# Kernel tuning notes

Measured on AMD Instinct MI355X. Metric: run time of the kernel, lower is better.

## Reference

```python
import jax, jax.numpy as jnp
import numpy as np

B, IN, H, OUT, E = 8192, 1024, 4096, 1024, 8
HG = H // 2  # gating hidden

def setup_inputs() -> dict:
    key = jax.random.key(0)
    ks = jax.random.split(key, 9)
    s_in = 1.0 / np.sqrt(IN)
    s_h = 1.0 / np.sqrt(H)
    s_hg = 1.0 / np.sqrt(HG)
    return {
        "x": jax.random.normal(ks[0], (B, IN), jnp.float32),
        # gating MLP: Linear(IN,HG) -> ReLU -> Linear(HG,E) -> softmax
        "gw1": jax.random.uniform(ks[1], (IN, HG), jnp.float32, -s_in, s_in),
        "gb1": jax.random.uniform(ks[2], (HG,), jnp.float32, -s_in, s_in),
        "gw2": jax.random.uniform(ks[3], (HG, E), jnp.float32, -s_hg, s_hg),
        "gb2": jax.random.uniform(ks[4], (E,), jnp.float32, -s_hg, s_hg),
        # experts: E x (Linear(IN,H) -> ReLU -> Linear(H,OUT))
        "ew1": jax.random.uniform(ks[5], (E, IN, H), jnp.float32, -s_in, s_in),
        "eb1": jax.random.uniform(ks[6], (E, H), jnp.float32, -s_in, s_in),
        "ew2": jax.random.uniform(ks[7], (E, H, OUT), jnp.float32, -s_h, s_h),
        "eb2": jax.random.uniform(ks[8], (E, OUT), jnp.float32, -s_h, s_h),
    }

def reference(x, gw1, gb1, gw2, gb2, ew1, eb1, ew2, eb2):
    # Gating network (dropout is a no-op in eval)
    gh = jax.nn.relu(x @ gw1 + gb1)                       # [B, HG]
    gates = jax.nn.softmax(gh @ gw2 + gb2, axis=1)        # [B, E]
    # All experts run on the full batch
    h = jax.nn.relu(jnp.einsum('bi,eih->beh', x, ew1) + eb1[None])  # [B, E, H]
    eo = jnp.einsum('beh,eho->beo', h, ew2) + eb2[None]             # [B, E, OUT]
    # Gate-weighted combine: (stacked * gates[...,None]).sum(dim=1)
    combined = jnp.einsum('beo,be->bo', eo, gates)        # [B, OUT]
    return combined
```

## Files before the change

### kernel.cpp

```cpp
#include <hip/hip_runtime.h>


#define DI __device__ __forceinline__

typedef _Float16 f16;
typedef _Float16 f16x8 __attribute__((ext_vector_type(8)));
typedef float f32x4 __attribute__((ext_vector_type(4)));

constexpr int BSZ  = 8192;
constexpr int IND  = 1024;
constexpr int HID  = 4096;
constexpr int OUTD = 1024;
constexpr int NE   = 8;
constexpr int HGD  = 2048;

__global__ __launch_bounds__(256) void conv_f32_f16_kernel(
    const float* __restrict__ in, f16* __restrict__ out)
{
    size_t i = ((size_t)blockIdx.x * 256 + threadIdx.x) * 8;
    const float4* p = (const float4*)(in + i);
    float4 a = p[0], b = p[1];
    f16x8 v = {(f16)a.x, (f16)a.y, (f16)a.z, (f16)a.w,
               (f16)b.x, (f16)b.y, (f16)b.z, (f16)b.w};
    *(f16x8*)(out + i) = v;
}

__global__ __launch_bounds__(256) void transpose_f32_f16_kernel(
    const float* __restrict__ W, f16* __restrict__ Wt, int K, int N)
{
    W  += (size_t)blockIdx.z * K * N;
    Wt += (size_t)blockIdx.z * N * K;
    __shared__ float t[64][65];
    int n0 = blockIdx.x * 64, k0 = blockIdx.y * 64;
    int tx = threadIdx.x & 63, ty = threadIdx.x >> 6;
#pragma unroll
    for (int i = 0; i < 16; i++) {
        int k = i * 4 + ty;
        t[k][tx] = W[(size_t)(k0 + k) * N + n0 + tx];
    }
    __syncthreads();
#pragma unroll
    for (int i = 0; i < 16; i++) {
        int n = i * 4 + ty;
        Wt[(size_t)(n0 + n) * K + k0 + tx] = (f16)t[tx][n];
    }
}

DI void gload_lds16(const void* g, void* l)
{
    typedef const __attribute__((address_space(1))) unsigned int as1_t;
    typedef __attribute__((address_space(3))) unsigned int as3_t;
    __builtin_amdgcn_global_load_lds(
        (as1_t*)(unsigned long long)(__SIZE_TYPE__)g,
        (as3_t*)(unsigned int)(__SIZE_TYPE__)l,
        16, 0, 0);
}

#define SYNC_HEAD                                                              \
    __builtin_amdgcn_sched_barrier(0);                                         \
    __builtin_amdgcn_s_barrier();                                              \
    asm volatile("s_waitcnt lgkmcnt(0)" ::: "memory");                         \
    __builtin_amdgcn_sched_barrier(0);
#define SYNC_HEAD_T8                                                           \
    __builtin_amdgcn_sched_barrier(0);                                         \
    asm volatile("s_waitcnt lgkmcnt(8)");                                      \
    __builtin_amdgcn_s_barrier();                                              \
    asm volatile("s_waitcnt lgkmcnt(0)" ::: "memory");                         \
    __builtin_amdgcn_sched_barrier(0);
#define SYNC_TAIL                                                              \
    __builtin_amdgcn_sched_barrier(0);                                         \
    __builtin_amdgcn_s_barrier();                                              \
    asm volatile("" ::: "memory");

template <bool RELU>
__global__ __launch_bounds__(512, 2) void gemm256_kernel(
    const f16* __restrict__ A, const f16* __restrict__ Bt,
    const float* __restrict__ bias, f16* __restrict__ Cptr,
    int M, int N, int K)
{
    constexpr int BM = 256, BN = 256, BK = 64;
    constexpr int AT = BM * BK * 2, BT = BN * BK * 2;
    __shared__ __align__(16) f16 sA[2][BM * BK];
    __shared__ __align__(16) f16 sB[2][BN * BK];
    const char* sAc = (const char*)sA;
    const char* sBc = (const char*)sB;

    const int tid = threadIdx.x, wid = tid >> 6, lane = tid & 63;
    const int wm = wid >> 2, wn = wid & 3;
    const int nwg = gridDim.x, bid = blockIdx.x;
    const int wg = (bid & 7) * (nwg >> 3) + (bid >> 3);
    const int gx = N / BN;
    const size_t bm = (size_t)(wg / gx) * BM;
    const size_t bn = (size_t)(wg % gx) * BN;

    f32x4 acc[8][4] = {};

    const int rho  = tid >> 3;
    const int slot = (((tid & 7) << 4) ^ (((tid >> 3) & 7) << 4));
    const f16* pA = A  + (bm + rho) * (size_t)K + (slot >> 1);
    const f16* pB = Bt + (bn + rho) * (size_t)K + (slot >> 1);

    auto stA = [&](int b, int q, int T) {
        gload_lds16(pA + ((size_t)q * 64) * K + (size_t)T * BK,
                    (char*)sAc + b * AT + q * 8192 + wid * 1024);
    };
    auto stB = [&](int b, int q, int T) {
        gload_lds16(pB + ((size_t)q * 64) * K + (size_t)T * BK,
                    (char*)sBc + b * BT + q * 8192 + wid * 1024);
    };

    int offA0[8], offB0[4];
#pragma unroll
    for (int f = 0; f < 8; f++) {
        int r = wm * 128 + f * 16 + (lane & 15);
        offA0[f] = r * 128 + ((((lane >> 4) << 4)) ^ ((r & 7) << 4));
    }
#pragma unroll
    for (int f = 0; f < 4; f++) {
        int r = wn * 64 + f * 16 + (lane & 15);
        offB0[f] = r * 128 + ((((lane >> 4) << 4)) ^ ((r & 7) << 4));
    }

    f16x8 av[4][2], bv0[2][2], bv1[2][2];

#define LDAQ(B, MH)                                                            \
    _Pragma("unroll") for (int f = 0; f < 4; f++)                              \
    _Pragma("unroll") for (int kc = 0; kc < 2; kc++)                           \
        av[f][kc] = *(const f16x8*)(sAc + (B) * AT + (offA0[(MH)*4+f] ^ (kc << 6)));
#define LDBH(B, NH, BV)                                                        \
    _Pragma("unroll") for (int f = 0; f < 2; f++)                              \
    _Pragma("unroll") for (int kc = 0; kc < 2; kc++)                           \
        BV[f][kc] = *(const f16x8*)(sBc + (B) * BT + (offB0[(NH)*2+f] ^ (kc << 6)));
#define QUAD(MH, NH, BV)                                                       \
    __builtin_amdgcn_s_setprio(1);                                             \
    _Pragma("unroll") for (int f = 0; f < 4; f++)                              \
    _Pragma("unroll") for (int g = 0; g < 2; g++)                              \
    _Pragma("unroll") for (int kc = 0; kc < 2; kc++)                           \
        acc[(MH)*4+f][(NH)*2+g] = __builtin_amdgcn_mfma_f32_16x16x32_f16(      \
            av[f][kc], BV[g][kc], acc[(MH)*4+f][(NH)*2+g], 0, 0, 0);           \
    __builtin_amdgcn_s_setprio(0);

    const int NT = K / BK, NI = NT / 2;

    stA(0,0,0); stA(0,2,0); stB(0,0,0); stB(0,1,0); stB(0,2,0); stB(0,3,0);
    stA(0,1,0); stA(0,3,0);
    stA(1,0,1); stA(1,2,1); stB(1,0,1); stB(1,1,1); stB(1,2,1); stB(1,3,1);
    asm volatile("s_waitcnt vmcnt(6)");
    __builtin_amdgcn_s_barrier();
    asm volatile("" ::: "memory");

    for (int i = 0; i < NI - 1; ++i) {
        const int t = 2 * i;
        LDAQ(0, 0) LDBH(0, 0, bv0)
        stA(1, 1, t + 1); stA(1, 3, t + 1);
        SYNC_HEAD_T8
        QUAD(0, 0, bv0)
        SYNC_TAIL
        LDBH(0, 1, bv1)
        stA(0, 0, t + 2); stA(0, 2, t + 2);
        SYNC_HEAD
        QUAD(0, 1, bv1)
        SYNC_TAIL
        LDAQ(0, 1)
        stB(0, 0, t + 2); stB(0, 1, t + 2);
        SYNC_HEAD
        QUAD(1, 1, bv1)
        SYNC_TAIL
        stB(0, 2, t + 2); stB(0, 3, t + 2);
        SYNC_HEAD
        QUAD(1, 0, bv0)
        asm volatile("s_waitcnt vmcnt(6)");
        SYNC_TAIL
        LDAQ(1, 0) LDBH(1, 0, bv0)
        stA(0, 1, t + 2); stA(0, 3, t + 2);
        SYNC_HEAD_T8
        QUAD(0, 0, bv0)
        SYNC_TAIL
        LDBH(1, 1, bv1)
        stA(1, 0, t + 3); stA(1, 2, t + 3);
        SYNC_HEAD
        QUAD(0, 1, bv1)
        SYNC_TAIL
        LDAQ(1, 1)
        stB(1, 0, t + 3); stB(1, 1, t + 3);
        SYNC_HEAD
        QUAD(1, 1, bv1)
        SYNC_TAIL
        stB(1, 2, t + 3); stB(1, 3, t + 3);
        SYNC_HEAD
        QUAD(1, 0, bv0)
        asm volatile("s_waitcnt vmcnt(6)");
        SYNC_TAIL
    }
    {
        LDAQ(0, 0) LDBH(0, 0, bv0)
        stA(1, 1, NT - 1); stA(1, 3, NT - 1);
        SYNC_HEAD_T8
        QUAD(0, 0, bv0)
        SYNC_TAIL
        LDBH(0, 1, bv1)
        SYNC_HEAD
        QUAD(0, 1, bv1)
        SYNC_TAIL
        LDAQ(0, 1)
        SYNC_HEAD
        QUAD(1, 1, bv1)
        SYNC_TAIL
        SYNC_HEAD
        QUAD(1, 0, bv0)
        asm volatile("s_waitcnt vmcnt(0)");
        SYNC_TAIL
        LDAQ(1, 0) LDBH(1, 0, bv0)
        SYNC_HEAD
        QUAD(0, 0, bv0)
        SYNC_TAIL
        LDBH(1, 1, bv1)
        SYNC_HEAD
        QUAD(0, 1, bv1)
        SYNC_TAIL
        LDAQ(1, 1)
        SYNC_HEAD
        QUAD(1, 1, bv1)
        SYNC_TAIL
        SYNC_HEAD
        QUAD(1, 0, bv0)
        SYNC_TAIL
    }
#undef LDAQ
#undef LDBH
#undef QUAD

    const size_t row0 = bm + (size_t)wm * 128;
    const int col0 = (int)bn + wn * 64;
    const int c0 = lane & 15, r0 = (lane >> 4) * 4;
#pragma unroll
    for (int fm = 0; fm < 8; fm++)
#pragma unroll
        for (int r = 0; r < 4; r++) {
            const size_t row = row0 + fm * 16 + r0 + r;
#pragma unroll
            for (int n = 0; n < 4; n++) {
                const size_t col = (size_t)col0 + n * 16 + c0;
                float v = acc[fm][n][r] + bias[col];
                if constexpr (RELU) v = fmaxf(v, 0.0f);
                Cptr[row * (size_t)N + col] = (f16)v;
            }
        }
}

template <bool ACCUM>
__global__ __launch_bounds__(512, 2) void gemmO_kernel(
    const f16* __restrict__ A, const f16* __restrict__ Bt,
    const float* __restrict__ bias, const float* __restrict__ gate,
    float* __restrict__ Cptr, int M, int N, int K)
{
    constexpr int BM = 256, BN = 128, BK = 64;
    constexpr int AT = BM * BK * 2, BT = BN * BK * 2;
    __shared__ __align__(16) f16 sA[2][BM * BK];
    __shared__ __align__(16) f16 sB[2][BN * BK];
    const char* sAc = (const char*)sA;
    const char* sBc = (const char*)sB;

    const int tid = threadIdx.x, wid = tid >> 6, lane = tid & 63;
    const int wm = wid >> 2, wn = wid & 3;
    const int nwg = gridDim.x, bid = blockIdx.x;
    const int wg = (bid & 7) * (nwg >> 3) + (bid >> 3);
    const int gx = N / BN;
    const size_t bm = (size_t)(wg / gx) * BM;
    const size_t bn = (size_t)(wg % gx) * BN;

    f32x4 acc[8][2] = {};

    const int rho  = tid >> 3;
    const int slot = (((tid & 7) << 4) ^ (((tid >> 3) & 7) << 4));
    const f16* pA = A  + (bm + rho) * (size_t)K + (slot >> 1);
    const f16* pB = Bt + (bn + rho) * (size_t)K + (slot >> 1);

    auto stA = [&](int b, int q, int T) {
        gload_lds16(pA + ((size_t)q * 64) * K + (size_t)T * BK,
                    (char*)sAc + b * AT + q * 8192 + wid * 1024);
    };
    auto stB = [&](int b, int q, int T) {
        gload_lds16(pB + ((size_t)q * 64) * K + (size_t)T * BK,
                    (char*)sBc + b * BT + q * 8192 + wid * 1024);
    };

    int offA0[8], offB0[2];
#pragma unroll
    for (int f = 0; f < 8; f++) {
        int r = wm * 128 + f * 16 + (lane & 15);
        offA0[f] = r * 128 + ((((lane >> 4) << 4)) ^ ((r & 7) << 4));
    }
#pragma unroll
    for (int f = 0; f < 2; f++) {
        int r = wn * 32 + f * 16 + (lane & 15);
        offB0[f] = r * 128 + ((((lane >> 4) << 4)) ^ ((r & 7) << 4));
    }

    f16x8 av[4], bv[2][2];

#define LDA4(B, MH, KC)                                                        \
    _Pragma("unroll") for (int f = 0; f < 4; f++)                              \
        av[f] = *(const f16x8*)(sAc + (B) * AT + (offA0[(MH)*4+f] ^ ((KC) << 6)));
#define LDBA(B)                                                                \
    _Pragma("unroll") for (int f = 0; f < 2; f++)                              \
    _Pragma("unroll") for (int kc = 0; kc < 2; kc++)                           \
        bv[f][kc] = *(const f16x8*)(sBc + (B) * BT + (offB0[f] ^ (kc << 6)));
#define OCT(MH, KC)                                                            \
    __builtin_amdgcn_s_setprio(1);                                             \
    _Pragma("unroll") for (int f = 0; f < 4; f++)                              \
    _Pragma("unroll") for (int g = 0; g < 2; g++)                              \
        acc[(MH)*4+f][g] = __builtin_amdgcn_mfma_f32_16x16x32_f16(             \
            av[f], bv[g][KC], acc[(MH)*4+f][g], 0, 0, 0);                      \
    __builtin_amdgcn_s_setprio(0);

    const int NT = K / BK, NI = NT / 2;

    stA(0,0,0); stA(0,2,0); stB(0,0,0); stB(0,1,0); stA(0,1,0); stA(0,3,0);
    stA(1,0,1); stA(1,2,1); stB(1,0,1); stB(1,1,1);
    asm volatile("s_waitcnt vmcnt(4)");
    __builtin_amdgcn_s_barrier();
    asm volatile("" ::: "memory");

    for (int i = 0; i < NI - 1; ++i) {
        const int t = 2 * i;
        LDA4(0, 0, 0) LDBA(0)
        stA(1, 1, t + 1); stA(1, 3, t + 1);
        SYNC_HEAD
        OCT(0, 0)
        SYNC_TAIL
        LDA4(0, 0, 1)
        SYNC_HEAD
        OCT(0, 1)
        SYNC_TAIL
        LDA4(0, 1, 0)
        stA(0, 0, t + 2); stA(0, 2, t + 2);
        SYNC_HEAD
        OCT(1, 0)
        SYNC_TAIL
        LDA4(0, 1, 1)
        stB(0, 0, t + 2); stB(0, 1, t + 2);
        SYNC_HEAD
        OCT(1, 1)
        asm volatile("s_waitcnt vmcnt(4)");
        SYNC_TAIL
        LDA4(1, 0, 0) LDBA(1)
        stA(0, 1, t + 2); stA(0, 3, t + 2);
        SYNC_HEAD
        OCT(0, 0)
        SYNC_TAIL
        LDA4(1, 0, 1)
        SYNC_HEAD
        OCT(0, 1)
        SYNC_TAIL
        LDA4(1, 1, 0)
        stA(1, 0, t + 3); stA(1, 2, t + 3);
        SYNC_HEAD
        OCT(1, 0)
        SYNC_TAIL
        LDA4(1, 1, 1)
        stB(1, 0, t + 3); stB(1, 1, t + 3);
        SYNC_HEAD
        OCT(1, 1)
        asm volatile("s_waitcnt vmcnt(4)");
        SYNC_TAIL
    }
    {
        LDA4(0, 0, 0) LDBA(0)
        stA(1, 1, NT - 1); stA(1, 3, NT - 1);
        SYNC_HEAD
        OCT(0, 0)
        SYNC_TAIL
        LDA4(0, 0, 1)
        SYNC_HEAD
        OCT(0, 1)
        SYNC_TAIL
        LDA4(0, 1, 0)
        SYNC_HEAD
        OCT(1, 0)
        SYNC_TAIL
        LDA4(0, 1, 1)
        SYNC_HEAD
        OCT(1, 1)
        asm volatile("s_waitcnt vmcnt(0)");
        SYNC_TAIL
        LDA4(1, 0, 0) LDBA(1)
        SYNC_HEAD
        OCT(0, 0)
        SYNC_TAIL
        LDA4(1, 0, 1)
        SYNC_HEAD
        OCT(0, 1)
        SYNC_TAIL
        LDA4(1, 1, 0)
        SYNC_HEAD
        OCT(1, 0)
        SYNC_TAIL
        LDA4(1, 1, 1)
        SYNC_HEAD
        OCT(1, 1)
        SYNC_TAIL
    }
#undef LDA4
#undef LDBA
#undef OCT

    const size_t row0 = bm + (size_t)wm * 128;
    const int col0 = (int)bn + wn * 32;
    const int c0 = lane & 15, r0 = (lane >> 4) * 4;
#pragma unroll
    for (int fm = 0; fm < 8; fm++)
#pragma unroll
        for (int r = 0; r < 4; r++) {
            const size_t row = row0 + fm * 16 + r0 + r;
            const float g = gate[row * NE];
#pragma unroll
            for (int n = 0; n < 2; n++) {
                const size_t col = (size_t)col0 + n * 16 + c0;
                float v = (acc[fm][n][r] + bias[col]) * g;
                float* p = Cptr + row * (size_t)N + col;
                *p = ACCUM ? (*p + v) : v;
            }
        }
}

__global__ __launch_bounds__(256) void gate_softmax_kernel(
    const f16* __restrict__ gh, const float* __restrict__ gw2,
    const float* __restrict__ gb2, float* __restrict__ gates)
{
    const int row  = blockIdx.x * 4 + (threadIdx.x >> 6);
    const int lane = threadIdx.x & 63;
    const f16* r = gh + (size_t)row * HGD;
    float acc[NE] = {};
    for (int kb = lane * 8; kb < HGD; kb += 512) {
        f16x8 v = *(const f16x8*)(r + kb);
#pragma unroll
        for (int j = 0; j < 8; j++) {
            float h = (float)v[j];
            const float* w = gw2 + (size_t)(kb + j) * NE;
#pragma unroll
            for (int e = 0; e < NE; e++) acc[e] = fmaf(h, w[e], acc[e]);
        }
    }
#pragma unroll
    for (int off = 32; off > 0; off >>= 1)
#pragma unroll
        for (int e = 0; e < NE; e++) acc[e] += __shfl_down(acc[e], off, 64);
    if (lane == 0) {
        float l[NE], m = -1e30f;
#pragma unroll
        for (int e = 0; e < NE; e++) { l[e] = acc[e] + gb2[e]; m = fmaxf(m, l[e]); }
        float s = 0.f;
#pragma unroll
        for (int e = 0; e < NE; e++) { l[e] = expf(l[e] - m); s += l[e]; }
        float inv = 1.0f / s;
#pragma unroll
        for (int e = 0; e < NE; e++) gates[(size_t)row * NE + e] = l[e] * inv;
    }
}

extern "C" void kernel_launch(void* const* d_in, const int* in_sizes, int n_in,
                              void* d_out, int out_size, void* d_ws, size_t ws_size,
                              hipStream_t stream)
{
    const float* x   = (const float*)d_in[0];
    const float* gw1 = (const float*)d_in[1];
    const float* gb1 = (const float*)d_in[2];
    const float* gw2 = (const float*)d_in[3];
    const float* gb2 = (const float*)d_in[4];
    const float* ew1 = (const float*)d_in[5];
    const float* eb1 = (const float*)d_in[6];
    const float* ew2 = (const float*)d_in[7];
    const float* eb2 = (const float*)d_in[8];
    float* out = (float*)d_out;

    const size_t SZ_GATES = 256 << 10;
    const size_t SZ_X16   = (size_t)BSZ * IND * 2;
    const size_t SZ_WBUF  = (size_t)HID * IND * 2;
    const size_t SZ_W1ALL = (size_t)NE * HID * IND * 2;
    const size_t SZ_W2ALL = (size_t)NE * OUTD * HID * 2;
    const size_t SZ_HBUF  = (size_t)BSZ * HID * 2;
    const size_t NEED_A = SZ_GATES + SZ_X16 + SZ_W1ALL + SZ_W2ALL + SZ_HBUF;
    const size_t NEED_B = SZ_GATES + SZ_X16 + SZ_WBUF + SZ_W2ALL + SZ_HBUF;

    char* p = (char*)d_ws;
    float* gates = (float*)p;  p += SZ_GATES;
    f16* x16 = (f16*)p;        p += SZ_X16;

    conv_f32_f16_kernel<<<(BSZ * IND) / (256 * 8), 256, 0, stream>>>(x, x16);

    if (ws_size >= NEED_A) {
        f16* w1all = (f16*)p;  p += SZ_W1ALL;
        f16* w2all = (f16*)p;  p += SZ_W2ALL;
        f16* hbuf  = (f16*)p;
        f16* gh    = hbuf;

        transpose_f32_f16_kernel<<<dim3(HGD / 64, IND / 64, 1), 256, 0, stream>>>(
            gw1, w1all, IND, HGD);
        gemm256_kernel<true><<<(HGD / 256) * (BSZ / 256), 512, 0, stream>>>(
            x16, w1all, gb1, gh, BSZ, HGD, IND);
        gate_softmax_kernel<<<BSZ / 4, 256, 0, stream>>>(gh, gw2, gb2, gates);

        transpose_f32_f16_kernel<<<dim3(HID / 64, IND / 64, NE), 256, 0, stream>>>(
            ew1, w1all, IND, HID);
        transpose_f32_f16_kernel<<<dim3(OUTD / 64, HID / 64, NE), 256, 0, stream>>>(
            ew2, w2all, HID, OUTD);

        for (int e = 0; e < NE; e++) {
            gemm256_kernel<true><<<(HID / 256) * (BSZ / 256), 512, 0, stream>>>(
                x16, w1all + (size_t)e * HID * IND, eb1 + (size_t)e * HID,
                hbuf, BSZ, HID, IND);
            if (e == 0)
                gemmO_kernel<false><<<(OUTD / 128) * (BSZ / 256), 512, 0, stream>>>(
                    hbuf, w2all + (size_t)e * OUTD * HID, eb2 + (size_t)e * OUTD,
                    gates + e, out, BSZ, OUTD, HID);
            else
                gemmO_kernel<true><<<(OUTD / 128) * (BSZ / 256), 512, 0, stream>>>(
                    hbuf, w2all + (size_t)e * OUTD * HID, eb2 + (size_t)e * OUTD,
                    gates + e, out, BSZ, OUTD, HID);
        }
    } else if (ws_size >= NEED_B) {
        f16* wbuf  = (f16*)p;  p += SZ_WBUF;
        f16* w2all = (f16*)p;  p += SZ_W2ALL;
        f16* hbuf  = (f16*)p;
        f16* gh    = hbuf;

        transpose_f32_f16_kernel<<<dim3(HGD / 64, IND / 64, 1), 256, 0, stream>>>(
            gw1, wbuf, IND, HGD);
        gemm256_kernel<true><<<(HGD / 256) * (BSZ / 256), 512, 0, stream>>>(
            x16, wbuf, gb1, gh, BSZ, HGD, IND);
        gate_softmax_kernel<<<BSZ / 4, 256, 0, stream>>>(gh, gw2, gb2, gates);

        transpose_f32_f16_kernel<<<dim3(OUTD / 64, HID / 64, NE), 256, 0, stream>>>(
            ew2, w2all, HID, OUTD);

        for (int e = 0; e < NE; e++) {
            transpose_f32_f16_kernel<<<dim3(HID / 64, IND / 64, 1), 256, 0, stream>>>(
                ew1 + (size_t)e * IND * HID, wbuf, IND, HID);
            gemm256_kernel<true><<<(HID / 256) * (BSZ / 256), 512, 0, stream>>>(
                x16, wbuf, eb1 + (size_t)e * HID, hbuf, BSZ, HID, IND);
            if (e == 0)
                gemmO_kernel<false><<<(OUTD / 128) * (BSZ / 256), 512, 0, stream>>>(
                    hbuf, w2all + (size_t)e * OUTD * HID, eb2 + (size_t)e * OUTD,
                    gates + e, out, BSZ, OUTD, HID);
            else
                gemmO_kernel<true><<<(OUTD / 128) * (BSZ / 256), 512, 0, stream>>>(
                    hbuf, w2all + (size_t)e * OUTD * HID, eb2 + (size_t)e * OUTD,
                    gates + e, out, BSZ, OUTD, HID);
        }
    } else {
        f16* wbuf = (f16*)p;   p += SZ_WBUF;
        f16* hbuf = (f16*)p;
        f16* gh   = hbuf;

        transpose_f32_f16_kernel<<<dim3(HGD / 64, IND / 64, 1), 256, 0, stream>>>(
            gw1, wbuf, IND, HGD);
        gemm256_kernel<true><<<(HGD / 256) * (BSZ / 256), 512, 0, stream>>>(
            x16, wbuf, gb1, gh, BSZ, HGD, IND);
        gate_softmax_kernel<<<BSZ / 4, 256, 0, stream>>>(gh, gw2, gb2, gates);

        for (int e = 0; e < NE; e++) {
            transpose_f32_f16_kernel<<<dim3(HID / 64, IND / 64, 1), 256, 0, stream>>>(
                ew1 + (size_t)e * IND * HID, wbuf, IND, HID);
            gemm256_kernel<true><<<(HID / 256) * (BSZ / 256), 512, 0, stream>>>(
                x16, wbuf, eb1 + (size_t)e * HID, hbuf, BSZ, HID, IND);

            transpose_f32_f16_kernel<<<dim3(OUTD / 64, HID / 64, 1), 256, 0, stream>>>(
                ew2 + (size_t)e * HID * OUTD, wbuf, HID, OUTD);
            if (e == 0)
                gemmO_kernel<false><<<(OUTD / 128) * (BSZ / 256), 512, 0, stream>>>(
                    hbuf, wbuf, eb2 + (size_t)e * OUTD, gates + e, out,
                    BSZ, OUTD, HID);
            else
                gemmO_kernel<true><<<(OUTD / 128) * (BSZ / 256), 512, 0, stream>>>(
                    hbuf, wbuf, eb2 + (size_t)e * OUTD, gates + e, out,
                    BSZ, OUTD, HID);
        }
    }
}
```

Before: 1.388 ms.

## Group experts into batched launches with gate-scaled hidden and concatenated-K output GEMM

Up-projection GEMMs for G experts (4 or 2, depending on workspace size) now run as one launch over blockIdx.z. Each writes ReLU(hidden) already multiplied by its gate into a wide [B, G*H] buffer. The down-projection then runs one GEMM with K=G*H against the experts' W2 matrices laid side by side, folding the gate-weighted biases into the epilogue. This cuts launches and the read-modify-write passes over the fp32 output from 8 to NE/G. The cost is a larger hidden workspace and fp16 rounding of gate-scaled activations.

```diff
diff --git a/kernel.cpp b/kernel.cpp
--- a/kernel.cpp
+++ b/kernel.cpp
@@ -26,10 +26,12 @@
 }
 
 __global__ __launch_bounds__(256) void transpose_f32_f16_kernel(
-    const float* __restrict__ W, f16* __restrict__ Wt, int K, int N)
+    const float* __restrict__ W, f16* __restrict__ Wt, int K, int N,
+    int ldo, size_t zstride, int kostep)
 {
-    W  += (size_t)blockIdx.z * K * N;
-    Wt += (size_t)blockIdx.z * N * K;
+    const int z = blockIdx.z;
+    W += (size_t)z * K * N;
+    f16* base = Wt + (size_t)z * zstride + (size_t)z * kostep;
     __shared__ float t[64][65];
     int n0 = blockIdx.x * 64, k0 = blockIdx.y * 64;
     int tx = threadIdx.x & 63, ty = threadIdx.x >> 6;
@@ -42,7 +44,7 @@
 #pragma unroll
     for (int i = 0; i < 16; i++) {
         int n = i * 4 + ty;
-        Wt[(size_t)(n0 + n) * K + k0 + tx] = (f16)t[tx][n];
+        base[(size_t)(n0 + n) * ldo + k0 + tx] = (f16)t[tx][n];
     }
 }
 
@@ -72,11 +74,11 @@
     __builtin_amdgcn_s_barrier();                                              \
     asm volatile("" ::: "memory");
 
-template <bool RELU>
+template <bool RELU, bool GSCALE>
 __global__ __launch_bounds__(512, 2) void gemm256_kernel(
     const f16* __restrict__ A, const f16* __restrict__ Bt,
-    const float* __restrict__ bias, f16* __restrict__ Cptr,
-    int M, int N, int K)
+    const float* __restrict__ bias, const float* __restrict__ gate,
+    f16* __restrict__ Cptr, int M, int N, int K, int ldc, int e0)
 {
     constexpr int BM = 256, BN = 256, BK = 64;
     constexpr int AT = BM * BK * 2, BT = BN * BK * 2;
@@ -84,6 +86,10 @@
     __shared__ __align__(16) f16 sB[2][BN * BK];
     const char* sAc = (const char*)sA;
     const char* sBc = (const char*)sB;
+
+    const int z = blockIdx.z;
+    Bt   += (size_t)z * N * K;
+    bias += (size_t)z * N;
 
     const int tid = threadIdx.x, wid = tid >> 6, lane = tid & 63;
     const int wm = wid >> 2, wn = wid & 3;
@@ -233,26 +239,30 @@
     const size_t row0 = bm + (size_t)wm * 128;
     const int col0 = (int)bn + wn * 64;
     const int c0 = lane & 15, r0 = (lane >> 4) * 4;
+    f16* Cz = Cptr + (size_t)z * N;
 #pragma unroll
     for (int fm = 0; fm < 8; fm++)
 #pragma unroll
         for (int r = 0; r < 4; r++) {
             const size_t row = row0 + fm * 16 + r0 + r;
+            float g = 1.0f;
+            if constexpr (GSCALE) g = gate[row * NE + e0 + z];
 #pragma unroll
             for (int n = 0; n < 4; n++) {
                 const size_t col = (size_t)col0 + n * 16 + c0;
                 float v = acc[fm][n][r] + bias[col];
                 if constexpr (RELU) v = fmaxf(v, 0.0f);
-                Cptr[row * (size_t)N + col] = (f16)v;
+                if constexpr (GSCALE) v *= g;
+                Cz[row * (size_t)ldc + col] = (f16)v;
             }
         }
 }
 
-template <bool ACCUM>
+template <bool ACCUM, int GN>
 __global__ __launch_bounds__(512, 2) void gemmO_kernel(
     const f16* __restrict__ A, const f16* __restrict__ Bt,
     const float* __restrict__ bias, const float* __restrict__ gate,
-    float* __restrict__ Cptr, int M, int N, int K)
+    float* __restrict__ Cptr, int M, int N, int K, int ldb, int e0)
 {
     constexpr int BM = 256, BN = 128, BK = 64;
     constexpr int AT = BM * BK * 2, BT = BN * BK * 2;
@@ -273,15 +283,15 @@
 
     const int rho  = tid >> 3;
     const int slot = (((tid & 7) << 4) ^ (((tid >> 3) & 7) << 4));
-    const f16* pA = A  + (bm + rho) * (size_t)K + (slot >> 1);
-    const f16* pB = Bt + (bn + rho) * (size_t)K + (slot >> 1);
+    const f16* pA = A  + (bm + rho) * (size_t)K   + (slot >> 1);
+    const f16* pB = Bt + (bn + rho) * (size_t)ldb + (slot >> 1);
 
     auto stA = [&](int b, int q, int T) {
         gload_lds16(pA + ((size_t)q * 64) * K + (size_t)T * BK,
                     (char*)sAc + b * AT + q * 8192 + wid * 1024);
     };
     auto stB = [&](int b, int q, int T) {
-        gload_lds16(pB + ((size_t)q * 64) * K + (size_t)T * BK,
+        gload_lds16(pB + ((size_t)q * 64) * ldb + (size_t)T * BK,
                     (char*)sBc + b * BT + q * 8192 + wid * 1024);
     };
 
@@ -413,13 +423,30 @@
 #pragma unroll
         for (int r = 0; r < 4; r++) {
             const size_t row = row0 + fm * 16 + r0 + r;
-            const float g = gate[row * NE];
-#pragma unroll
-            for (int n = 0; n < 2; n++) {
-                const size_t col = (size_t)col0 + n * 16 + c0;
-                float v = (acc[fm][n][r] + bias[col]) * g;
-                float* p = Cptr + row * (size_t)N + col;
-                *p = ACCUM ? (*p + v) : v;
+            if constexpr (GN == 0) {
+                const float g = gate[row * NE];
+#pragma unroll
+                for (int n = 0; n < 2; n++) {
+                    const size_t col = (size_t)col0 + n * 16 + c0;
+                    float v = (acc[fm][n][r] + bias[col]) * g;
+                    float* p = Cptr + row * (size_t)N + col;
+                    *p = ACCUM ? (*p + v) : v;
+                }
+            } else {
+                float gv[GN];
+#pragma unroll
+                for (int j = 0; j < GN; j++) gv[j] = gate[row * NE + e0 + j];
+#pragma unroll
+                for (int n = 0; n < 2; n++) {
+                    const size_t col = (size_t)col0 + n * 16 + c0;
+                    float bb = 0.f;
+#pragma unroll
+                    for (int j = 0; j < GN; j++)
+                        bb = fmaf(gv[j], bias[(size_t)(e0 + j) * N + col], bb);
+                    float v = acc[fm][n][r] + bb;
+                    float* p = Cptr + row * (size_t)N + col;
+                    *p = ACCUM ? (*p + v) : v;
+                }
             }
         }
 }
@@ -479,9 +506,12 @@
     const size_t SZ_WBUF  = (size_t)HID * IND * 2;
     const size_t SZ_W1ALL = (size_t)NE * HID * IND * 2;
     const size_t SZ_W2ALL = (size_t)NE * OUTD * HID * 2;
-    const size_t SZ_HBUF  = (size_t)BSZ * HID * 2;
-    const size_t NEED_A = SZ_GATES + SZ_X16 + SZ_W1ALL + SZ_W2ALL + SZ_HBUF;
-    const size_t NEED_B = SZ_GATES + SZ_X16 + SZ_WBUF + SZ_W2ALL + SZ_HBUF;
+    const size_t SZ_HB1   = (size_t)BSZ * HID * 2;
+    const size_t BASE     = SZ_GATES + SZ_X16 + SZ_W1ALL + SZ_W2ALL;
+    const size_t NEED_G4  = BASE + 4 * SZ_HB1;
+    const size_t NEED_G2  = BASE + 2 * SZ_HB1;
+    const size_t NEED_G1  = BASE + 1 * SZ_HB1;
+    const size_t NEED_C   = SZ_GATES + SZ_X16 + SZ_WBUF + SZ_HB1;
 
     char* p = (char*)d_ws;
     float* gates = (float*)p;  p += SZ_GATES;
@@ -489,64 +519,85 @@
 
     conv_f32_f16_kernel<<<(BSZ * IND) / (256 * 8), 256, 0, stream>>>(x, x16);
 
-    if (ws_size >= NEED_A) {
+    if (ws_size >= NEED_G2) {
+        const int G = (ws_size >= NEED_G4) ? 4 : 2;
+        f16* w1all = (f16*)p;  p += SZ_W1ALL;
+        f16* w2cat = (f16*)p;  p += SZ_W2ALL;
+        f16* hbufG = (f16*)p;
+        f16* gh    = hbufG;
+
+        transpose_f32_f16_kernel<<<dim3(HGD / 64, IND / 64, 1), 256, 0, stream>>>(
+            gw1, w1all, IND, HGD, IND, 0, 0);
+        gemm256_kernel<true, false>
+            <<<dim3((HGD / 256) * (BSZ / 256), 1, 1), 512, 0, stream>>>(
+                x16, w1all, gb1, nullptr, gh, BSZ, HGD, IND, HGD, 0);
+        gate_softmax_kernel<<<BSZ / 4, 256, 0, stream>>>(gh, gw2, gb2, gates);
+
+        transpose_f32_f16_kernel<<<dim3(HID / 64, IND / 64, NE), 256, 0, stream>>>(
+            ew1, w1all, IND, HID, IND, (size_t)HID * IND, 0);
+        transpose_f32_f16_kernel<<<dim3(OUTD / 64, HID / 64, NE), 256, 0, stream>>>(
+            ew2, w2cat, HID, OUTD, NE * HID, 0, HID);
+
+        for (int g = 0; g < NE / G; g++) {
+            gemm256_kernel<true, true>
+                <<<dim3((HID / 256) * (BSZ / 256), 1, G), 512, 0, stream>>>(
+                    x16, w1all + (size_t)g * G * HID * IND, eb1 + g * G * HID,
+                    gates, hbufG, BSZ, HID, IND, G * HID, g * G);
+            if (G == 4) {
+                if (g == 0)
+                    gemmO_kernel<false, 4>
+                        <<<(OUTD / 128) * (BSZ / 256), 512, 0, stream>>>(
+                            hbufG, w2cat + (size_t)g * G * HID, eb2, gates, out,
+                            BSZ, OUTD, G * HID, NE * HID, g * G);
+                else
+                    gemmO_kernel<true, 4>
+                        <<<(OUTD / 128) * (BSZ / 256), 512, 0, stream>>>(
+                            hbufG, w2cat + (size_t)g * G * HID, eb2, gates, out,
+                            BSZ, OUTD, G * HID, NE * HID, g * G);
+            } else {
+                if (g == 0)
+                    gemmO_kernel<false, 2>
+                        <<<(OUTD / 128) * (BSZ / 256), 512, 0, stream>>>(
+                            hbufG, w2cat + (size_t)g * G * HID, eb2, gates, out,
+                            BSZ, OUTD, G * HID, NE * HID, g * G);
+                else
+                    gemmO_kernel<true, 2>
+                        <<<(OUTD / 128) * (BSZ / 256), 512, 0, stream>>>(
+                            hbufG, w2cat + (size_t)g * G * HID, eb2, gates, out,
+                            BSZ, OUTD, G * HID, NE * HID, g * G);
+            }
+        }
+    } else if (ws_size >= NEED_G1) {
         f16* w1all = (f16*)p;  p += SZ_W1ALL;
         f16* w2all = (f16*)p;  p += SZ_W2ALL;
         f16* hbuf  = (f16*)p;
         f16* gh    = hbuf;
 
         transpose_f32_f16_kernel<<<dim3(HGD / 64, IND / 64, 1), 256, 0, stream>>>(
-            gw1, w1all, IND, HGD);
-        gemm256_kernel<true><<<(HGD / 256) * (BSZ / 256), 512, 0, stream>>>(
-            x16, w1all, gb1, gh, BSZ, HGD, IND);
+            gw1, w1all, IND, HGD, IND, 0, 0);
+        gemm256_kernel<true, false>
+            <<<dim3((HGD / 256) * (BSZ / 256), 1, 1), 512, 0, stream>>>(
+                x16, w1all, gb1, nullptr, gh, BSZ, HGD, IND, HGD, 0);
         gate_softmax_kernel<<<BSZ / 4, 256, 0, stream>>>(gh, gw2, gb2, gates);
 
         transpose_f32_f16_kernel<<<dim3(HID / 64, IND / 64, NE), 256, 0, stream>>>(
-            ew1, w1all, IND, HID);
+            ew1, w1all, IND, HID, IND, (size_t)HID * IND, 0);
         transpose_f32_f16_kernel<<<dim3(OUTD / 64, HID / 64, NE), 256, 0, stream>>>(
-            ew2, w2all, HID, OUTD);
+            ew2, w2all, HID, OUTD, HID, (size_t)OUTD * HID, 0);
 
         for (int e = 0; e < NE; e++) {
-            gemm256_kernel<true><<<(HID / 256) * (BSZ / 256), 512, 0, stream>>>(
-                x16, w1all + (size_t)e * HID * IND, eb1 + (size_t)e * HID,
-                hbuf, BSZ, HID, IND);
+            gemm256_kernel<true, false>
+                <<<dim3((HID / 256) * (BSZ / 256), 1, 1), 512, 0, stream>>>(
+                    x16, w1all + (size_t)e * HID * IND, eb1 + (size_t)e * HID,
+                    nullptr, hbuf, BSZ, HID, IND, HID, 0);
             if (e == 0)
-                gemmO_kernel<false><<<(OUTD / 128) * (BSZ / 256), 512, 0, stream>>>(
+                gemmO_kernel<false, 0><<<(OUTD / 128) * (BSZ / 256), 512, 0, stream>>>(
                     hbuf, w2all + (size_t)e * OUTD * HID, eb2 + (size_t)e * OUTD,
-                    gates + e, out, BSZ, OUTD, HID);
+                    gates + e, out, BSZ, OUTD, HID, HID, 0);
             else
-                gemmO_kernel<true><<<(OUTD / 128) * (BSZ / 256), 512, 0, stream>>>(
+                gemmO_kernel<true, 0><<<(OUTD / 128) * (BSZ / 256), 512, 0, stream>>>(
                     hbuf, w2all + (size_t)e * OUTD * HID, eb2 + (size_t)e * OUTD,
-                    gates + e, out, BSZ, OUTD, HID);
-        }
-    } else if (ws_size >= NEED_B) {
-        f16* wbuf  = (f16*)p;  p += SZ_WBUF;
-        f16* w2all = (f16*)p;  p += SZ_W2ALL;
-        f16* hbuf  = (f16*)p;
-        f16* gh    = hbuf;
-
-        transpose_f32_f16_kernel<<<dim3(HGD / 64, IND / 64, 1), 256, 0, stream>>>(
-            gw1, wbuf, IND, HGD);
-        gemm256_kernel<true><<<(HGD / 256) * (BSZ / 256), 512, 0, stream>>>(
-            x16, wbuf, gb1, gh, BSZ, HGD, IND);
-        gate_softmax_kernel<<<BSZ / 4, 256, 0, stream>>>(gh, gw2, gb2, gates);
-
-        transpose_f32_f16_kernel<<<dim3(OUTD / 64, HID / 64, NE), 256, 0, stream>>>(
-            ew2, w2all, HID, OUTD);
-
-        for (int e = 0; e < NE; e++) {
-            transpose_f32_f16_kernel<<<dim3(HID / 64, IND / 64, 1), 256, 0, stream>>>(
-                ew1 + (size_t)e * IND * HID, wbuf, IND, HID);
-            gemm256_kernel<true><<<(HID / 256) * (BSZ / 256), 512, 0, stream>>>(
-                x16, wbuf, eb1 + (size_t)e * HID, hbuf, BSZ, HID, IND);
-            if (e == 0)
-                gemmO_kernel<false><<<(OUTD / 128) * (BSZ / 256), 512, 0, stream>>>(
-                    hbuf, w2all + (size_t)e * OUTD * HID, eb2 + (size_t)e * OUTD,
-                    gates + e, out, BSZ, OUTD, HID);
-            else
-                gemmO_kernel<true><<<(OUTD / 128) * (BSZ / 256), 512, 0, stream>>>(
-                    hbuf, w2all + (size_t)e * OUTD * HID, eb2 + (size_t)e * OUTD,
-                    gates + e, out, BSZ, OUTD, HID);
+                    gates + e, out, BSZ, OUTD, HID, HID, 0);
         }
     } else {
         f16* wbuf = (f16*)p;   p += SZ_WBUF;
@@ -554,27 +605,30 @@
         f16* gh   = hbuf;
 
         transpose_f32_f16_kernel<<<dim3(HGD / 64, IND / 64, 1), 256, 0, stream>>>(
-            gw1, wbuf, IND, HGD);
-        gemm256_kernel<true><<<(HGD / 256) * (BSZ / 256), 512, 0, stream>>>(
-            x16, wbuf, gb1, gh, BSZ, HGD, IND);
+            gw1, wbuf, IND, HGD, IND, 0, 0);
+        gemm256_kernel<true, false>
+            <<<dim3((HGD / 256) * (BSZ / 256), 1, 1), 512, 0, stream>>>(
+                x16, wbuf, gb1, nullptr, gh, BSZ, HGD, IND, HGD, 0);
         gate_softmax_kernel<<<BSZ / 4, 256, 0, stream>>>(gh, gw2, gb2, gates);
 
         for (int e = 0; e < NE; e++) {
             transpose_f32_f16_kernel<<<dim3(HID / 64, IND / 64, 1), 256, 0, stream>>>(
-                ew1 + (size_t)e * IND * HID, wbuf, IND, HID);
-            gemm256_kernel<true><<<(HID / 256) * (BSZ / 256), 512, 0, stream>>>(
-                x16, wbuf, eb1 + (size_t)e * HID, hbuf, BSZ, HID, IND);
+                ew1 + (size_t)e * IND * HID, wbuf, IND, HID, IND, 0, 0);
+            gemm256_kernel<true, false>
+                <<<dim3((HID / 256) * (BSZ / 256), 1, 1), 512, 0, stream>>>(
+                    x16, wbuf, eb1 + (size_t)e * HID, nullptr, hbuf,
+                    BSZ, HID, IND, HID, 0);
 
             transpose_f32_f16_kernel<<<dim3(OUTD / 64, HID / 64, 1), 256, 0, stream>>>(
-                ew2 + (size_t)e * HID * OUTD, wbuf, HID, OUTD);
+                ew2 + (size_t)e * HID * OUTD, wbuf, HID, OUTD, HID, 0, 0);
             if (e == 0)
-                gemmO_kernel<false><<<(OUTD / 128) * (BSZ / 256), 512, 0, stream>>>(
+                gemmO_kernel<false, 0><<<(OUTD / 128) * (BSZ / 256), 512, 0, stream>>>(
                     hbuf, wbuf, eb2 + (size_t)e * OUTD, gates + e, out,
-                    BSZ, OUTD, HID);
+                    BSZ, OUTD, HID, HID, 0);
             else
-                gemmO_kernel<true><<<(OUTD / 128) * (BSZ / 256), 512, 0, stream>>>(
+                gemmO_kernel<true, 0><<<(OUTD / 128) * (BSZ / 256), 512, 0, stream>>>(
                     hbuf, wbuf, eb2 + (size_t)e * OUTD, gates + e, out,
-                    BSZ, OUTD, HID);
+                    BSZ, OUTD, HID, HID, 0);
         }
     }
 }
```

After: 1.319 ms. -5.0%, faster.
